# Kernel optimization log

Measured on AMD Instinct MI355X. Metric: run time of the kernel, lower is better.

Reference implementation:

```python
import jax, jax.numpy as jnp
import numpy as np

NEG_INF = -1e10  # matches the -10000000000.0 additive mask in the torch source


def setup_inputs() -> dict:
    key = jax.random.key(0)
    k1, k2, k3, k4 = jax.random.split(key, 4)
    bs, h, S, d = 4, 16, 2048, 64
    bs_h = bs * h
    query = jax.random.normal(k1, (bs_h, S, d), dtype=jnp.float32)
    key_t = jax.random.normal(k2, (bs_h, S, d), dtype=jnp.float32)
    value = jax.random.normal(k3, (bs_h, S, d), dtype=jnp.float32)
    attn_mask = jax.random.randint(k4, (bs, S), 0, 2).astype(jnp.int32)
    return {"query": query, "key": key_t, "value": value,
            "attn_mask": attn_mask, "decod_mask": 1}


def reference(query, key, value, attn_mask, decod_mask):
    bs_h, K, d_k = key.shape
    Q = query.shape[1]
    bs = attn_mask.shape[0]
    h = bs_h // bs

    # scores: [bs_h, Q, K]
    scores = jnp.einsum('bqd,bkd->bqk', query, key) / jnp.sqrt(
        jnp.asarray(d_k, dtype=query.dtype))

    # padding mask: positions where attn_mask == 0 get -1e10.
    # torch repeats the [bs, Q, K] mask h times along the batch axis
    # (order: [mask; mask; ...]), i.e. batch index b in bs_h maps to b % bs.
    pad = (attn_mask == 0).astype(scores.dtype) * NEG_INF  # [bs, K]
    scores = (scores.reshape(h, bs, Q, K) + pad[None, :, None, :]).reshape(bs_h, Q, K)

    if decod_mask is not None:
        causal = jnp.triu(jnp.full((Q, K), NEG_INF, dtype=scores.dtype), k=1)
        scores = scores + causal[None, :, :]

    attn = jax.nn.softmax(scores, axis=-1)
    # dropout p=0.0 -> identity
    return jnp.einsum('bqk,bkd->bqd', attn, value)
```

## Files before the change

kernel.cpp:

```cpp
#include <hip/hip_runtime.h>
#include <hip/hip_bf16.h>

#define S_LEN 2048
#define DH 64
#define NBATCH 4
#define LOG2E 1.44269504088896f
#define SCL2E 0.18033688011112042f
#define PADC  (-1.44269504088896e10f)
#define NEG_BIG -1e10f
#define NEG_CAUSAL -3.0e38f

typedef __attribute__((ext_vector_type(8))) short short8;
typedef __attribute__((ext_vector_type(4))) float floatx4;
typedef __attribute__((ext_vector_type(4))) unsigned uintx4;

__device__ inline float fast_exp2(float x) {
#if __has_builtin(__builtin_amdgcn_exp2f)
  return __builtin_amdgcn_exp2f(x);
#else
  return exp2f(x);
#endif
}

__device__ inline short f2bf(float x) {
  union { float f; unsigned u; } v; v.f = x;
  unsigned r = v.u + 0x7fffu + ((v.u >> 16) & 1u);
  return (short)(r >> 16);
}

__device__ inline short8 pack8(float4 a, float4 b) {
  short8 r;
  r[0] = f2bf(a.x); r[1] = f2bf(a.y); r[2] = f2bf(a.z); r[3] = f2bf(a.w);
  r[4] = f2bf(b.x); r[5] = f2bf(b.y); r[6] = f2bf(b.z); r[7] = f2bf(b.w);
  return r;
}

__device__ inline unsigned packhi(unsigned hi, unsigned lo) {
#if __has_builtin(__builtin_amdgcn_perm)
  return __builtin_amdgcn_perm(hi, lo, 0x07060302u);
#else
  return (hi & 0xFFFF0000u) | (lo >> 16);
#endif
}

#define MFMA32(a, b, c) __builtin_amdgcn_mfma_f32_16x16x32_bf16(a, b, c, 0, 0, 0)

__global__ void prep_kv(const float* __restrict__ Kg, const float* __restrict__ Vg,
                        short8* __restrict__ Kf, short8* __restrict__ Vf) {
  const int gid = (int)blockIdx.x;
  if (gid < 4096) {
    const int idx = gid * 256 + (int)threadIdx.x;
    const int lane = idx & 63;
    const int t = idx >> 6;
    const int nt = t & 3, ks = (t >> 2) & 1;
    const int kt = (t >> 3) & 31;
    const int bh = t >> 8;
    const int c = lane & 15, g = lane >> 4;
    const float* src = Kg + ((size_t)bh * S_LEN + kt * 64 + nt * 16 + c) * DH + ks * 32 + g * 8;
    float4 a = *(const float4*)src;
    float4 b = *(const float4*)(src + 4);
    Kf[idx] = pack8(a, b);
  } else {
    const int idx = (gid - 4096) * 256 + (int)threadIdx.x;
    const int lane = idx & 63;
    const int t = idx >> 6;
    const int dt = t & 3, nt2 = (t >> 2) & 1;
    const int kt = (t >> 3) & 31;
    const int bh = t >> 8;
    const int c = lane & 15, g = lane >> 4;
    const int key0 = kt * 64 + nt2 * 32 + g * 4;
    const float* src = Vg + ((size_t)bh * S_LEN + key0) * DH + dt * 16 + c;
    short8 r;
#pragma unroll
    for (int j = 0; j < 4; ++j) r[j] = f2bf(src[(size_t)j * DH]);
#pragma unroll
    for (int j = 0; j < 4; ++j) r[4 + j] = f2bf(src[(size_t)(16 + j) * DH]);
    Vf[idx] = r;
  }
}

__global__ __launch_bounds__(256, 2) void flash_fwd2(
    const float* __restrict__ Qg, const int* __restrict__ maskg,
    const short8* __restrict__ KfB, const short8* __restrict__ VfB,
    float* __restrict__ Og)
{
  const int bh = blockIdx.x;
  const int qt = 15 - (int)blockIdx.y;
  const int b  = bh & (NBATCH - 1);
  const int tid = (int)threadIdx.x;
  const int w = tid >> 6, lane = tid & 63;
  const int c = lane & 15, g = lane >> 4;
  const int qbase = qt * 128 + w * 32;

  const short8 ones = {0x3F80, 0x3F80, 0x3F80, 0x3F80, 0x3F80, 0x3F80, 0x3F80, 0x3F80};

  short8 qf[2][2];
#pragma unroll
  for (int s2 = 0; s2 < 2; ++s2) {
    const float* qp = Qg + ((size_t)bh * S_LEN + qbase + s2 * 16 + c) * DH + g * 8;
#pragma unroll
    for (int ks = 0; ks < 2; ++ks) {
      float4 a  = *(const float4*)(qp + ks * 32);
      float4 b4 = *(const float4*)(qp + ks * 32 + 4);
      qf[s2][ks] = pack8(a, b4);
    }
  }

  floatx4 acc[2][4];
  floatx4 acc_l[2];
#pragma unroll
  for (int s2 = 0; s2 < 2; ++s2) {
    acc_l[s2] = (floatx4){0.f, 0.f, 0.f, 0.f};
#pragma unroll
    for (int dt = 0; dt < 4; ++dt) acc[s2][dt] = (floatx4){0.f, 0.f, 0.f, 0.f};
  }

  const int ktmax = 2 * qt + 1;
  for (int kt = 0; kt <= ktmax; ++kt) {
    const short8* kfp = KfB + ((size_t)(bh * 32 + kt) * 8) * 64 + lane;
    short8 kf[2][4];
#pragma unroll
    for (int ks = 0; ks < 2; ++ks)
#pragma unroll
      for (int nt = 0; nt < 4; ++nt) kf[ks][nt] = kfp[(ks * 4 + nt) * 64];

    const short8* vfp = VfB + ((size_t)(bh * 32 + kt) * 8) * 64 + lane;
    short8 vf[2][4];
#pragma unroll
    for (int nt2 = 0; nt2 < 2; ++nt2)
#pragma unroll
      for (int dt = 0; dt < 4; ++dt) vf[nt2][dt] = vfp[(nt2 * 4 + dt) * 64];

    floatx4 padv[4];
#pragma unroll
    for (int nt = 0; nt < 4; ++nt) {
      int4 mv = *(const int4*)&maskg[b * S_LEN + kt * 64 + nt * 16 + g * 4];
      padv[nt][0] = mv.x ? 0.f : PADC;
      padv[nt][1] = mv.y ? 0.f : PADC;
      padv[nt][2] = mv.z ? 0.f : PADC;
      padv[nt][3] = mv.w ? 0.f : PADC;
    }

#pragma unroll
    for (int s2 = 0; s2 < 2; ++s2) {
      if (kt * 64 > qbase + s2 * 16 + 15) continue;
      floatx4 st[4];
#pragma unroll
      for (int nt = 0; nt < 4; ++nt) {
        floatx4 cc = (floatx4){0.f, 0.f, 0.f, 0.f};
        cc = MFMA32(kf[0][nt], qf[s2][0], cc);
        cc = MFMA32(kf[1][nt], qf[s2][1], cc);
        st[nt] = cc;
      }
      const int q = qbase + s2 * 16 + c;
      const bool causal = (kt * 64 + 63) > (qbase + s2 * 16);
      unsigned pu[4][4];
#pragma unroll
      for (int nt = 0; nt < 4; ++nt) {
#pragma unroll
        for (int r = 0; r < 4; ++r) {
          float arg = fmaf(st[nt][r], SCL2E, padv[nt][r]);
          if (causal) {
            const int key = kt * 64 + nt * 16 + g * 4 + r;
            arg = (key > q) ? NEG_CAUSAL : arg;
          }
          pu[nt][r] = __float_as_uint(fast_exp2(arg)) + 0x8000u;
        }
      }
      short8 pP[2];
#pragma unroll
      for (int nt2 = 0; nt2 < 2; ++nt2) {
        uintx4 wv;
        wv[0] = packhi(pu[2 * nt2][1],     pu[2 * nt2][0]);
        wv[1] = packhi(pu[2 * nt2][3],     pu[2 * nt2][2]);
        wv[2] = packhi(pu[2 * nt2 + 1][1], pu[2 * nt2 + 1][0]);
        wv[3] = packhi(pu[2 * nt2 + 1][3], pu[2 * nt2 + 1][2]);
        pP[nt2] = __builtin_bit_cast(short8, wv);
      }
#pragma unroll
      for (int nt2 = 0; nt2 < 2; ++nt2) {
        acc_l[s2] = MFMA32(pP[nt2], ones, acc_l[s2]);
#pragma unroll
        for (int dt = 0; dt < 4; ++dt)
          acc[s2][dt] = MFMA32(pP[nt2], vf[nt2][dt], acc[s2][dt]);
      }
    }
  }

#pragma unroll
  for (int s2 = 0; s2 < 2; ++s2) {
    float rr[4];
#pragma unroll
    for (int r = 0; r < 4; ++r) rr[r] = 1.f / acc_l[s2][r];
#pragma unroll
    for (int dt = 0; dt < 4; ++dt)
#pragma unroll
      for (int r = 0; r < 4; ++r)
        Og[((size_t)bh * S_LEN + qbase + s2 * 16 + g * 4 + r) * DH + dt * 16 + c] =
            acc[s2][dt][r] * rr[r];
  }
}

__global__ __launch_bounds__(256, 2) void flash_fwd_lds(
    const float* __restrict__ Qg, const float* __restrict__ Kg,
    const float* __restrict__ Vg, const int* __restrict__ maskg,
    float* __restrict__ Og)
{
  const int qt  = blockIdx.x;
  const int bh  = blockIdx.y;
  const int b   = bh & (NBATCH - 1);
  const int tid = (int)threadIdx.x;
  const int w = tid >> 6, lane = tid & 63;
  const int g = lane >> 4, c = lane & 15;

  __shared__ __align__(16) short Ks[64 * 72];
  __shared__ __align__(16) short Vt[64 * 72];
  __shared__ __align__(16) short Ps[4][32 * 72];

  short8 qf[2][2];
#pragma unroll
  for (int s2 = 0; s2 < 2; ++s2) {
    const float* qp = Qg + ((size_t)bh * S_LEN + qt * 128 + w * 32 + s2 * 16 + c) * DH + g * 8;
#pragma unroll
    for (int ks = 0; ks < 2; ++ks) {
      float4 a  = *(const float4*)(qp + ks * 32);
      float4 bq = *(const float4*)(qp + ks * 32 + 4);
      qf[s2][ks] = pack8(a, bq);
    }
  }

  floatx4 acc[2][4];
  float mrow[2][4], lrow[2][4];
#pragma unroll
  for (int s2 = 0; s2 < 2; ++s2) {
#pragma unroll
    for (int i = 0; i < 4; ++i) acc[s2][i] = (floatx4){0.f, 0.f, 0.f, 0.f};
#pragma unroll
    for (int r = 0; r < 4; ++r) { mrow[s2][r] = -3.4e38f; lrow[s2][r] = 0.f; }
  }

  const int rstage = tid >> 2;
  const int dstage = (tid & 3) * 16;
  const int ktmax = 2 * qt + 1;

  for (int kt = 0; kt <= ktmax; ++kt) {
    __syncthreads();
    {
      const size_t rowbase = ((size_t)bh * S_LEN + kt * 64 + rstage) * DH + dstage;
      const float* kp = Kg + rowbase;
      const float* vp = Vg + rowbase;
      float4 k0 = *(const float4*)kp;       float4 k1 = *(const float4*)(kp + 4);
      float4 k2 = *(const float4*)(kp + 8); float4 k3 = *(const float4*)(kp + 12);
      *(short8*)&Ks[rstage * 72 + dstage]     = pack8(k0, k1);
      *(short8*)&Ks[rstage * 72 + dstage + 8] = pack8(k2, k3);
      float4 v0 = *(const float4*)vp;       float4 v1 = *(const float4*)(vp + 4);
      float4 v2 = *(const float4*)(vp + 8); float4 v3 = *(const float4*)(vp + 12);
      float vv[16] = {v0.x, v0.y, v0.z, v0.w, v1.x, v1.y, v1.z, v1.w,
                      v2.x, v2.y, v2.z, v2.w, v3.x, v3.y, v3.z, v3.w};
#pragma unroll
      for (int i = 0; i < 16; ++i) Vt[(dstage + i) * 72 + rstage] = f2bf(vv[i]);
    }
    __syncthreads();

    float padv[4];
#pragma unroll
    for (int nt = 0; nt < 4; ++nt)
      padv[nt] = (maskg[b * S_LEN + kt * 64 + nt * 16 + c] != 0) ? 0.f : NEG_BIG;

    short8 kf[2][4];
#pragma unroll
    for (int ks = 0; ks < 2; ++ks)
#pragma unroll
      for (int nt = 0; nt < 4; ++nt)
        kf[ks][nt] = *(const short8*)&Ks[(nt * 16 + c) * 72 + ks * 32 + g * 8];

    bool act[2];
#pragma unroll
    for (int s2 = 0; s2 < 2; ++s2)
      act[s2] = (kt * 64) <= (qt * 128 + w * 32 + s2 * 16 + 15);

#pragma unroll
    for (int s2 = 0; s2 < 2; ++s2) {
      if (!act[s2]) continue;
      floatx4 sv[4];
#pragma unroll
      for (int nt = 0; nt < 4; ++nt) {
        floatx4 cc = (floatx4){0.f, 0.f, 0.f, 0.f};
        cc = MFMA32(qf[s2][0], kf[0][nt], cc);
        cc = MFMA32(qf[s2][1], kf[1][nt], cc);
        sv[nt] = cc;
      }
      const int qrow0 = qt * 128 + w * 32 + s2 * 16 + g * 4;
#pragma unroll
      for (int nt = 0; nt < 4; ++nt) {
        const int key = kt * 64 + nt * 16 + c;
#pragma unroll
        for (int r = 0; r < 4; ++r) {
          float s = sv[nt][r] * 0.125f + padv[nt];
          if (key > qrow0 + r) s = NEG_CAUSAL;
          sv[nt][r] = s;
        }
      }
#pragma unroll
      for (int r = 0; r < 4; ++r) {
        float mx = fmaxf(fmaxf(sv[0][r], sv[1][r]), fmaxf(sv[2][r], sv[3][r]));
        mx = fmaxf(mx, __shfl_xor(mx, 1));
        mx = fmaxf(mx, __shfl_xor(mx, 2));
        mx = fmaxf(mx, __shfl_xor(mx, 4));
        mx = fmaxf(mx, __shfl_xor(mx, 8));
        const float mold = mrow[s2][r];
        const float mnew = fmaxf(mold, mx);
        const float corr = fast_exp2((mold - mnew) * LOG2E);
        float ps = 0.f;
#pragma unroll
        for (int nt = 0; nt < 4; ++nt) {
          float p = fast_exp2((sv[nt][r] - mnew) * LOG2E);
          sv[nt][r] = p;
          ps += p;
        }
        ps += __shfl_xor(ps, 1);
        ps += __shfl_xor(ps, 2);
        ps += __shfl_xor(ps, 4);
        ps += __shfl_xor(ps, 8);
        lrow[s2][r] = lrow[s2][r] * corr + ps;
        mrow[s2][r] = mnew;
#pragma unroll
        for (int dt = 0; dt < 4; ++dt) acc[s2][dt][r] *= corr;
      }
#pragma unroll
      for (int nt = 0; nt < 4; ++nt)
#pragma unroll
        for (int r = 0; r < 4; ++r)
          Ps[w][(s2 * 16 + g * 4 + r) * 72 + nt * 16 + c] = f2bf(sv[nt][r]);
    }

#pragma unroll
    for (int ks = 0; ks < 2; ++ks) {
      short8 pf0 = {}, pf1 = {};
      if (act[0]) pf0 = *(const short8*)&Ps[w][c * 72 + ks * 32 + g * 8];
      if (act[1]) pf1 = *(const short8*)&Ps[w][(16 + c) * 72 + ks * 32 + g * 8];
#pragma unroll
      for (int dt = 0; dt < 4; ++dt) {
        short8 vfr = *(const short8*)&Vt[(dt * 16 + c) * 72 + ks * 32 + g * 8];
        if (act[0]) acc[0][dt] = MFMA32(pf0, vfr, acc[0][dt]);
        if (act[1]) acc[1][dt] = MFMA32(pf1, vfr, acc[1][dt]);
      }
    }
  }

#pragma unroll
  for (int s2 = 0; s2 < 2; ++s2) {
    float rl[4];
#pragma unroll
    for (int r = 0; r < 4; ++r) rl[r] = 1.f / lrow[s2][r];
    const size_t obase = ((size_t)bh * S_LEN + qt * 128 + w * 32 + s2 * 16 + g * 4) * DH + c;
#pragma unroll
    for (int dt = 0; dt < 4; ++dt)
#pragma unroll
      for (int r = 0; r < 4; ++r)
        Og[obase + (size_t)r * DH + dt * 16] = acc[s2][dt][r] * rl[r];
  }
}

__global__ void fixup(const float* __restrict__ Vg, const int* __restrict__ maskg,
                      float* __restrict__ Og)
{
  const int bh = blockIdx.x;
  const int b  = bh & (NBATCH - 1);
  const int tid = (int)threadIdx.x;
  __shared__ int sFirst;
  __shared__ float4 sRed[64][16];
  __shared__ int sCnt[64];
  if (tid == 0) sFirst = S_LEN;
  __syncthreads();
  for (int k = tid; k < S_LEN; k += 1024)
    if (maskg[b * S_LEN + k] != 0) atomicMin(&sFirst, k);
  __syncthreads();
  const int f = sFirst;
  if (f == 0) return;

  const int dq = tid & 15, kg = tid >> 4;
  float4 a = {0.f, 0.f, 0.f, 0.f}; int cnt = 0;
  for (int k = kg; k < S_LEN; k += 64) {
    if (maskg[b * S_LEN + k] != 0) {
      float4 v = *(const float4*)&Vg[((size_t)bh * S_LEN + k) * DH + dq * 4];
      a.x += v.x; a.y += v.y; a.z += v.z; a.w += v.w; cnt++;
    }
  }
  sRed[kg][dq] = a;
  if (dq == 0) sCnt[kg] = cnt;
  __syncthreads();
  if (tid < 64) {
    const int q4 = tid >> 2, e = tid & 3;
    float ms = 0.f; int n = 0;
#pragma unroll 4
    for (int i = 0; i < 64; ++i) {
      const float* p4 = (const float*)&sRed[i][q4];
      ms += p4[e];
      n += sCnt[i];
    }
    float pre = 0.f;
    for (int q = 0; q < f; ++q) {
      pre += Vg[((size_t)bh * S_LEN + q) * DH + tid];
      Og[((size_t)bh * S_LEN + q) * DH + tid] = (pre + ms) / (float)(q + 1 + n);
    }
  }
}

extern "C" void kernel_launch(void* const* d_in, const int* in_sizes, int n_in,
                              void* d_out, int out_size, void* d_ws, size_t ws_size,
                              hipStream_t stream) {
  const float* Q = (const float*)d_in[0];
  const float* K = (const float*)d_in[1];
  const float* V = (const float*)d_in[2];
  const int* mask = (const int*)d_in[3];
  float* O = (float*)d_out;

  const size_t KF_BYTES = (size_t)64 * S_LEN * DH * 2;
  if (ws_size >= 2 * KF_BYTES) {
    short8* Kf = (short8*)d_ws;
    short8* Vf = (short8*)((char*)d_ws + KF_BYTES);
    prep_kv<<<dim3(8192), dim3(256), 0, stream>>>(K, V, Kf, Vf);
    flash_fwd2<<<dim3(64, 16), dim3(256), 0, stream>>>(Q, mask, Kf, Vf, O);
  } else {
    flash_fwd_lds<<<dim3(16, 64), dim3(256), 0, stream>>>(Q, K, V, mask, O);
  }
  fixup<<<dim3(64), dim3(1024), 0, stream>>>(V, mask, O);
}
```

Before: 222.0 us.

## Double-buffer K/V tiles in LDS via async global_load_lds with MFMA priority hints

Each workgroup now stages its K/V tiles into double-buffered shared memory using global_load_lds. Each wave copies one quarter of the next tile while the current tile is computed from LDS, with a barrier per iteration. Before, every wave read the same K/V fragments directly from global memory. This is meant to remove the redundant global traffic across the four waves and to overlap the loads with compute. It also wraps the MFMA sections in s_setprio. The risks are the added barrier per tile, which is problematic with per-wave causal early-outs, and a possible missing vmcnt wait before the barrier. It also adds 32KB of LDS per block, which could affect occupancy. It is unclear whether flash_fwd2 is the kernel launched by default.

```diff
diff --git a/kernel.cpp b/kernel.cpp
--- a/kernel.cpp
+++ b/kernel.cpp
@@ -44,6 +44,19 @@
 }
 
 #define MFMA32(a, b, c) __builtin_amdgcn_mfma_f32_16x16x32_bf16(a, b, c, 0, 0, 0)
+
+typedef __attribute__((address_space(1))) void __gas1_v;
+typedef __attribute__((address_space(3))) void __gas3_v;
+__device__ __forceinline__ void gload16(const void* g, void* l) {
+  __builtin_amdgcn_global_load_lds((__gas1_v*)g, (__gas3_v*)l, 16, 0, 0);
+}
+
+__device__ __forceinline__ void stage_chunk(const short8* src_base, short8* dst_base,
+                                            int lane) {
+#pragma unroll
+  for (int i = 0; i < 4; ++i)
+    gload16((const void*)(src_base + i * 64 + lane), (void*)(dst_base + i * 64));
+}
 
 __global__ void prep_kv(const float* __restrict__ Kg, const float* __restrict__ Vg,
                         short8* __restrict__ Kf, short8* __restrict__ Vf) {
@@ -92,6 +105,9 @@
   const int c = lane & 15, g = lane >> 4;
   const int qbase = qt * 128 + w * 32;
 
+  __shared__ short8 sK[2][512];
+  __shared__ short8 sV[2][512];
+
   const short8 ones = {0x3F80, 0x3F80, 0x3F80, 0x3F80, 0x3F80, 0x3F80, 0x3F80, 0x3F80};
 
   short8 qf[2][2];
@@ -115,36 +131,56 @@
     for (int dt = 0; dt < 4; ++dt) acc[s2][dt] = (floatx4){0.f, 0.f, 0.f, 0.f};
   }
 
+  const short8* gsel = (w & 2) ? (VfB + (size_t)bh * 32 * 512)
+                               : (KfB + (size_t)bh * 32 * 512);
+  const int half = (w & 1) * 256;
+
   const int ktmax = 2 * qt + 1;
+
+  {
+    short8* dsel = (w & 2) ? sV[0] : sK[0];
+    stage_chunk(gsel + half, dsel + half, lane);
+  }
+  __syncthreads();
+
+  int cur = 0;
   for (int kt = 0; kt <= ktmax; ++kt) {
-    const short8* kfp = KfB + ((size_t)(bh * 32 + kt) * 8) * 64 + lane;
+    int4 mv[4];
+#pragma unroll
+    for (int nt = 0; nt < 4; ++nt)
+      mv[nt] = *(const int4*)&maskg[b * S_LEN + kt * 64 + nt * 16 + g * 4];
+
+    if (kt < ktmax) {
+      short8* dsel = (w & 2) ? sV[cur ^ 1] : sK[cur ^ 1];
+      stage_chunk(gsel + (size_t)(kt + 1) * 512 + half, dsel + half, lane);
+    }
+
+    floatx4 padv[4];
+#pragma unroll
+    for (int nt = 0; nt < 4; ++nt) {
+      padv[nt][0] = mv[nt].x ? 0.f : PADC;
+      padv[nt][1] = mv[nt].y ? 0.f : PADC;
+      padv[nt][2] = mv[nt].z ? 0.f : PADC;
+      padv[nt][3] = mv[nt].w ? 0.f : PADC;
+    }
+
     short8 kf[2][4];
 #pragma unroll
     for (int ks = 0; ks < 2; ++ks)
 #pragma unroll
-      for (int nt = 0; nt < 4; ++nt) kf[ks][nt] = kfp[(ks * 4 + nt) * 64];
-
-    const short8* vfp = VfB + ((size_t)(bh * 32 + kt) * 8) * 64 + lane;
+      for (int nt = 0; nt < 4; ++nt) kf[ks][nt] = sK[cur][(ks * 4 + nt) * 64 + lane];
+
     short8 vf[2][4];
 #pragma unroll
     for (int nt2 = 0; nt2 < 2; ++nt2)
 #pragma unroll
-      for (int dt = 0; dt < 4; ++dt) vf[nt2][dt] = vfp[(nt2 * 4 + dt) * 64];
-
-    floatx4 padv[4];
-#pragma unroll
-    for (int nt = 0; nt < 4; ++nt) {
-      int4 mv = *(const int4*)&maskg[b * S_LEN + kt * 64 + nt * 16 + g * 4];
-      padv[nt][0] = mv.x ? 0.f : PADC;
-      padv[nt][1] = mv.y ? 0.f : PADC;
-      padv[nt][2] = mv.z ? 0.f : PADC;
-      padv[nt][3] = mv.w ? 0.f : PADC;
-    }
+      for (int dt = 0; dt < 4; ++dt) vf[nt2][dt] = sV[cur][(nt2 * 4 + dt) * 64 + lane];
 
 #pragma unroll
     for (int s2 = 0; s2 < 2; ++s2) {
       if (kt * 64 > qbase + s2 * 16 + 15) continue;
       floatx4 st[4];
+      __builtin_amdgcn_s_setprio(1);
 #pragma unroll
       for (int nt = 0; nt < 4; ++nt) {
         floatx4 cc = (floatx4){0.f, 0.f, 0.f, 0.f};
@@ -152,6 +188,7 @@
         cc = MFMA32(kf[1][nt], qf[s2][1], cc);
         st[nt] = cc;
       }
+      __builtin_amdgcn_s_setprio(0);
       const int q = qbase + s2 * 16 + c;
       const bool causal = (kt * 64 + 63) > (qbase + s2 * 16);
       unsigned pu[4][4];
@@ -177,6 +214,7 @@
         wv[3] = packhi(pu[2 * nt2 + 1][3], pu[2 * nt2 + 1][2]);
         pP[nt2] = __builtin_bit_cast(short8, wv);
       }
+      __builtin_amdgcn_s_setprio(1);
 #pragma unroll
       for (int nt2 = 0; nt2 < 2; ++nt2) {
         acc_l[s2] = MFMA32(pP[nt2], ones, acc_l[s2]);
@@ -184,6 +222,12 @@
         for (int dt = 0; dt < 4; ++dt)
           acc[s2][dt] = MFMA32(pP[nt2], vf[nt2][dt], acc[s2][dt]);
       }
+      __builtin_amdgcn_s_setprio(0);
+    }
+
+    if (kt < ktmax) {
+      __syncthreads();
+      cur ^= 1;
     }
   }
 
```

After: 223.4 us. No clear change (+0.6%).

## Balance causal work per wave, double-buffer K fragments, fold masked V sums into prep

Applied to the files above, without the earlier changes.

Each wave now processes two 32-row query chunks taken from opposite ends of the sequence (widx and 63-widx), so causal work per wave is balanced and the grid halves. K fragments are double-buffered in registers, loading the next tile while the current one computes, and s_setprio is raised around the MFMA blocks. The masked-V column sums used by the fully-masked-row fixup are now accumulated with atomics inside prep_kv, replacing the heavier fixup kernel with a lighter fixup_write. The trade-offs are more register pressure, an extra zeroing launch, and float atomics whose summation order is nondeterministic.

```diff
diff --git a/kernel.cpp b/kernel.cpp
--- a/kernel.cpp
+++ b/kernel.cpp
@@ -45,8 +45,13 @@
 
 #define MFMA32(a, b, c) __builtin_amdgcn_mfma_f32_16x16x32_bf16(a, b, c, 0, 0, 0)
 
+__global__ void zero_sums(float* __restrict__ s) {
+  s[blockIdx.x * 256 + threadIdx.x] = 0.f;
+}
+
 __global__ void prep_kv(const float* __restrict__ Kg, const float* __restrict__ Vg,
-                        short8* __restrict__ Kf, short8* __restrict__ Vf) {
+                        short8* __restrict__ Kf, short8* __restrict__ Vf,
+                        const int* __restrict__ maskg, float* __restrict__ sums) {
   const int gid = (int)blockIdx.x;
   if (gid < 4096) {
     const int idx = gid * 256 + (int)threadIdx.x;
@@ -67,137 +72,208 @@
     const int dt = t & 3, nt2 = (t >> 2) & 1;
     const int kt = (t >> 3) & 31;
     const int bh = t >> 8;
+    const int b = bh & (NBATCH - 1);
     const int c = lane & 15, g = lane >> 4;
     const int key0 = kt * 64 + nt2 * 32 + g * 4;
     const float* src = Vg + ((size_t)bh * S_LEN + key0) * DH + dt * 16 + c;
+    int4 m0 = *(const int4*)&maskg[b * S_LEN + key0];
+    int4 m1 = *(const int4*)&maskg[b * S_LEN + key0 + 16];
     short8 r;
-#pragma unroll
-    for (int j = 0; j < 4; ++j) r[j] = f2bf(src[(size_t)j * DH]);
-#pragma unroll
-    for (int j = 0; j < 4; ++j) r[4 + j] = f2bf(src[(size_t)(16 + j) * DH]);
+    float s = 0.f;
+    {
+      float v0 = src[(size_t)0 * DH], v1 = src[(size_t)1 * DH];
+      float v2 = src[(size_t)2 * DH], v3 = src[(size_t)3 * DH];
+      r[0] = f2bf(v0); r[1] = f2bf(v1); r[2] = f2bf(v2); r[3] = f2bf(v3);
+      s += (m0.x ? v0 : 0.f) + (m0.y ? v1 : 0.f) + (m0.z ? v2 : 0.f) + (m0.w ? v3 : 0.f);
+    }
+    {
+      float v0 = src[(size_t)16 * DH], v1 = src[(size_t)17 * DH];
+      float v2 = src[(size_t)18 * DH], v3 = src[(size_t)19 * DH];
+      r[4] = f2bf(v0); r[5] = f2bf(v1); r[6] = f2bf(v2); r[7] = f2bf(v3);
+      s += (m1.x ? v0 : 0.f) + (m1.y ? v1 : 0.f) + (m1.z ? v2 : 0.f) + (m1.w ? v3 : 0.f);
+    }
     Vf[idx] = r;
-  }
-}
-
-__global__ __launch_bounds__(256, 2) void flash_fwd2(
+    s += __shfl_xor(s, 16);
+    s += __shfl_xor(s, 32);
+    if (lane < 16) atomicAdd(&sums[bh * 64 + dt * 16 + lane], s);
+  }
+}
+
+__device__ __forceinline__ void loadk(const short8* __restrict__ kbase, int kt,
+                                      int lane, short8 (&dst)[8]) {
+  const short8* p = kbase + ((size_t)kt * 8) * 64 + lane;
+#pragma unroll
+  for (int i = 0; i < 8; ++i) dst[i] = p[i * 64];
+}
+
+__device__ __forceinline__ void compute_tile(
+    int kt, int qbase, int b, int c, int g, int lane,
+    const short8 (&kf)[8], const short8 (&qf)[2][2], const short8& ones,
+    const int* __restrict__ maskg, const short8* __restrict__ vbase,
+    floatx4 (&acc)[2][4], floatx4 (&acc_l)[2])
+{
+  int4 mv[4];
+#pragma unroll
+  for (int nt = 0; nt < 4; ++nt)
+    mv[nt] = *(const int4*)&maskg[b * S_LEN + kt * 64 + nt * 16 + g * 4];
+
+  short8 vf[8];
+  {
+    const short8* vp = vbase + ((size_t)kt * 8) * 64 + lane;
+#pragma unroll
+    for (int i = 0; i < 8; ++i) vf[i] = vp[i * 64];
+  }
+
+  floatx4 padv[4];
+#pragma unroll
+  for (int nt = 0; nt < 4; ++nt) {
+    padv[nt][0] = mv[nt].x ? 0.f : PADC;
+    padv[nt][1] = mv[nt].y ? 0.f : PADC;
+    padv[nt][2] = mv[nt].z ? 0.f : PADC;
+    padv[nt][3] = mv[nt].w ? 0.f : PADC;
+  }
+
+#pragma unroll
+  for (int s2 = 0; s2 < 2; ++s2) {
+    if (kt * 64 > qbase + s2 * 16 + 15) continue;
+    floatx4 st[4];
+    __builtin_amdgcn_s_setprio(1);
+#pragma unroll
+    for (int nt = 0; nt < 4; ++nt) {
+      floatx4 cc = (floatx4){0.f, 0.f, 0.f, 0.f};
+      cc = MFMA32(kf[nt],     qf[s2][0], cc);
+      cc = MFMA32(kf[4 + nt], qf[s2][1], cc);
+      st[nt] = cc;
+    }
+    __builtin_amdgcn_s_setprio(0);
+    const int q = qbase + s2 * 16 + c;
+    const bool causal = (kt * 64 + 63) > (qbase + s2 * 16);
+    unsigned pu[4][4];
+#pragma unroll
+    for (int nt = 0; nt < 4; ++nt) {
+#pragma unroll
+      for (int r = 0; r < 4; ++r) {
+        float arg = fmaf(st[nt][r], SCL2E, padv[nt][r]);
+        if (causal) {
+          const int key = kt * 64 + nt * 16 + g * 4 + r;
+          arg = (key > q) ? NEG_CAUSAL : arg;
+        }
+        pu[nt][r] = __float_as_uint(fast_exp2(arg)) + 0x8000u;
+      }
+    }
+    short8 pP[2];
+#pragma unroll
+    for (int nt2 = 0; nt2 < 2; ++nt2) {
+      uintx4 wv;
+      wv[0] = packhi(pu[2 * nt2][1],     pu[2 * nt2][0]);
+      wv[1] = packhi(pu[2 * nt2][3],     pu[2 * nt2][2]);
+      wv[2] = packhi(pu[2 * nt2 + 1][1], pu[2 * nt2 + 1][0]);
+      wv[3] = packhi(pu[2 * nt2 + 1][3], pu[2 * nt2 + 1][2]);
+      pP[nt2] = __builtin_bit_cast(short8, wv);
+    }
+    __builtin_amdgcn_s_setprio(1);
+#pragma unroll
+    for (int nt2 = 0; nt2 < 2; ++nt2) {
+      acc_l[s2] = MFMA32(pP[nt2], ones, acc_l[s2]);
+#pragma unroll
+      for (int dt = 0; dt < 4; ++dt)
+        acc[s2][dt] = MFMA32(pP[nt2], vf[nt2 * 4 + dt], acc[s2][dt]);
+    }
+    __builtin_amdgcn_s_setprio(0);
+  }
+}
+
+__global__ __launch_bounds__(256, 2) void flash_fwd3(
     const float* __restrict__ Qg, const int* __restrict__ maskg,
     const short8* __restrict__ KfB, const short8* __restrict__ VfB,
     float* __restrict__ Og)
 {
   const int bh = blockIdx.x;
-  const int qt = 15 - (int)blockIdx.y;
   const int b  = bh & (NBATCH - 1);
   const int tid = (int)threadIdx.x;
   const int w = tid >> 6, lane = tid & 63;
+  const int widx = (int)blockIdx.y * 4 + w;
   const int c = lane & 15, g = lane >> 4;
-  const int qbase = qt * 128 + w * 32;
 
   const short8 ones = {0x3F80, 0x3F80, 0x3F80, 0x3F80, 0x3F80, 0x3F80, 0x3F80, 0x3F80};
-
-  short8 qf[2][2];
-#pragma unroll
-  for (int s2 = 0; s2 < 2; ++s2) {
-    const float* qp = Qg + ((size_t)bh * S_LEN + qbase + s2 * 16 + c) * DH + g * 8;
-#pragma unroll
-    for (int ks = 0; ks < 2; ++ks) {
-      float4 a  = *(const float4*)(qp + ks * 32);
-      float4 b4 = *(const float4*)(qp + ks * 32 + 4);
-      qf[s2][ks] = pack8(a, b4);
-    }
-  }
-
-  floatx4 acc[2][4];
-  floatx4 acc_l[2];
-#pragma unroll
-  for (int s2 = 0; s2 < 2; ++s2) {
-    acc_l[s2] = (floatx4){0.f, 0.f, 0.f, 0.f};
-#pragma unroll
-    for (int dt = 0; dt < 4; ++dt) acc[s2][dt] = (floatx4){0.f, 0.f, 0.f, 0.f};
-  }
-
-  const int ktmax = 2 * qt + 1;
-  for (int kt = 0; kt <= ktmax; ++kt) {
-    const short8* kfp = KfB + ((size_t)(bh * 32 + kt) * 8) * 64 + lane;
-    short8 kf[2][4];
-#pragma unroll
-    for (int ks = 0; ks < 2; ++ks)
-#pragma unroll
-      for (int nt = 0; nt < 4; ++nt) kf[ks][nt] = kfp[(ks * 4 + nt) * 64];
-
-    const short8* vfp = VfB + ((size_t)(bh * 32 + kt) * 8) * 64 + lane;
-    short8 vf[2][4];
-#pragma unroll
-    for (int nt2 = 0; nt2 < 2; ++nt2)
-#pragma unroll
-      for (int dt = 0; dt < 4; ++dt) vf[nt2][dt] = vfp[(nt2 * 4 + dt) * 64];
-
-    floatx4 padv[4];
-#pragma unroll
-    for (int nt = 0; nt < 4; ++nt) {
-      int4 mv = *(const int4*)&maskg[b * S_LEN + kt * 64 + nt * 16 + g * 4];
-      padv[nt][0] = mv.x ? 0.f : PADC;
-      padv[nt][1] = mv.y ? 0.f : PADC;
-      padv[nt][2] = mv.z ? 0.f : PADC;
-      padv[nt][3] = mv.w ? 0.f : PADC;
-    }
-
+  const short8* kbase = KfB + (size_t)bh * 32 * 8 * 64;
+  const short8* vbase = VfB + (size_t)bh * 32 * 8 * 64;
+
+#pragma unroll
+  for (int half = 0; half < 2; ++half) {
+    const int ch = half ? (63 - widx) : widx;
+    const int qbase = ch * 32;
+    const int ktmax = ch >> 1;
+
+    short8 qf[2][2];
 #pragma unroll
     for (int s2 = 0; s2 < 2; ++s2) {
-      if (kt * 64 > qbase + s2 * 16 + 15) continue;
-      floatx4 st[4];
-#pragma unroll
-      for (int nt = 0; nt < 4; ++nt) {
-        floatx4 cc = (floatx4){0.f, 0.f, 0.f, 0.f};
-        cc = MFMA32(kf[0][nt], qf[s2][0], cc);
-        cc = MFMA32(kf[1][nt], qf[s2][1], cc);
-        st[nt] = cc;
-      }
-      const int q = qbase + s2 * 16 + c;
-      const bool causal = (kt * 64 + 63) > (qbase + s2 * 16);
-      unsigned pu[4][4];
-#pragma unroll
-      for (int nt = 0; nt < 4; ++nt) {
-#pragma unroll
-        for (int r = 0; r < 4; ++r) {
-          float arg = fmaf(st[nt][r], SCL2E, padv[nt][r]);
-          if (causal) {
-            const int key = kt * 64 + nt * 16 + g * 4 + r;
-            arg = (key > q) ? NEG_CAUSAL : arg;
-          }
-          pu[nt][r] = __float_as_uint(fast_exp2(arg)) + 0x8000u;
-        }
-      }
-      short8 pP[2];
-#pragma unroll
-      for (int nt2 = 0; nt2 < 2; ++nt2) {
-        uintx4 wv;
-        wv[0] = packhi(pu[2 * nt2][1],     pu[2 * nt2][0]);
-        wv[1] = packhi(pu[2 * nt2][3],     pu[2 * nt2][2]);
-        wv[2] = packhi(pu[2 * nt2 + 1][1], pu[2 * nt2 + 1][0]);
-        wv[3] = packhi(pu[2 * nt2 + 1][3], pu[2 * nt2 + 1][2]);
-        pP[nt2] = __builtin_bit_cast(short8, wv);
-      }
-#pragma unroll
-      for (int nt2 = 0; nt2 < 2; ++nt2) {
-        acc_l[s2] = MFMA32(pP[nt2], ones, acc_l[s2]);
-#pragma unroll
-        for (int dt = 0; dt < 4; ++dt)
-          acc[s2][dt] = MFMA32(pP[nt2], vf[nt2][dt], acc[s2][dt]);
-      }
-    }
-  }
-
-#pragma unroll
-  for (int s2 = 0; s2 < 2; ++s2) {
-    float rr[4];
-#pragma unroll
-    for (int r = 0; r < 4; ++r) rr[r] = 1.f / acc_l[s2][r];
-#pragma unroll
-    for (int dt = 0; dt < 4; ++dt)
-#pragma unroll
-      for (int r = 0; r < 4; ++r)
-        Og[((size_t)bh * S_LEN + qbase + s2 * 16 + g * 4 + r) * DH + dt * 16 + c] =
-            acc[s2][dt][r] * rr[r];
+      const float* qp = Qg + ((size_t)bh * S_LEN + qbase + s2 * 16 + c) * DH + g * 8;
+#pragma unroll
+      for (int ks = 0; ks < 2; ++ks) {
+        float4 a  = *(const float4*)(qp + ks * 32);
+        float4 b4 = *(const float4*)(qp + ks * 32 + 4);
+        qf[s2][ks] = pack8(a, b4);
+      }
+    }
+
+    floatx4 acc[2][4];
+    floatx4 acc_l[2];
+#pragma unroll
+    for (int s2 = 0; s2 < 2; ++s2) {
+      acc_l[s2] = (floatx4){0.f, 0.f, 0.f, 0.f};
+#pragma unroll
+      for (int dt = 0; dt < 4; ++dt) acc[s2][dt] = (floatx4){0.f, 0.f, 0.f, 0.f};
+    }
+
+    short8 kfA[8], kfB_[8];
+    loadk(kbase, 0, lane, kfA);
+    for (int kt = 0; kt <= ktmax; kt += 2) {
+      const bool hasB = (kt + 1 <= ktmax);
+      if (hasB) loadk(kbase, kt + 1, lane, kfB_);
+      compute_tile(kt, qbase, b, c, g, lane, kfA, qf, ones, maskg, vbase, acc, acc_l);
+      if (hasB) {
+        if (kt + 2 <= ktmax) loadk(kbase, kt + 2, lane, kfA);
+        compute_tile(kt + 1, qbase, b, c, g, lane, kfB_, qf, ones, maskg, vbase, acc, acc_l);
+      }
+    }
+
+#pragma unroll
+    for (int s2 = 0; s2 < 2; ++s2) {
+      float rr[4];
+#pragma unroll
+      for (int r = 0; r < 4; ++r) rr[r] = 1.f / acc_l[s2][r];
+#pragma unroll
+      for (int dt = 0; dt < 4; ++dt)
+#pragma unroll
+        for (int r = 0; r < 4; ++r)
+          Og[((size_t)bh * S_LEN + qbase + s2 * 16 + g * 4 + r) * DH + dt * 16 + c] =
+              acc[s2][dt][r] * rr[r];
+    }
+  }
+}
+
+__global__ void fixup_write(const float* __restrict__ Vg, const int* __restrict__ maskg,
+                            const float* __restrict__ sums, float* __restrict__ Og)
+{
+  const int bh = blockIdx.x;
+  const int b  = bh & (NBATCH - 1);
+  const int d  = (int)threadIdx.x;
+  int fmin = S_LEN, n = 0;
+  for (int k = d; k < S_LEN; k += 64) {
+    if (maskg[b * S_LEN + k] != 0) { ++n; if (k < fmin) fmin = k; }
+  }
+#pragma unroll
+  for (int off = 1; off < 64; off <<= 1) {
+    fmin = min(fmin, __shfl_xor(fmin, off));
+    n += __shfl_xor(n, off);
+  }
+  if (fmin == 0) return;
+  const float ms = sums[bh * 64 + d];
+  float pre = 0.f;
+  for (int q = 0; q < fmin; ++q) {
+    pre += Vg[((size_t)bh * S_LEN + q) * DH + d];
+    Og[((size_t)bh * S_LEN + q) * DH + d] = (pre + ms) / (float)(q + 1 + n);
   }
 }
 
@@ -417,13 +493,17 @@
   float* O = (float*)d_out;
 
   const size_t KF_BYTES = (size_t)64 * S_LEN * DH * 2;
-  if (ws_size >= 2 * KF_BYTES) {
+  const size_t SUM_BYTES = (size_t)64 * 64 * sizeof(float);
+  if (ws_size >= 2 * KF_BYTES + SUM_BYTES) {
     short8* Kf = (short8*)d_ws;
     short8* Vf = (short8*)((char*)d_ws + KF_BYTES);
-    prep_kv<<<dim3(8192), dim3(256), 0, stream>>>(K, V, Kf, Vf);
-    flash_fwd2<<<dim3(64, 16), dim3(256), 0, stream>>>(Q, mask, Kf, Vf, O);
+    float* sums = (float*)((char*)d_ws + 2 * KF_BYTES);
+    zero_sums<<<dim3(16), dim3(256), 0, stream>>>(sums);
+    prep_kv<<<dim3(8192), dim3(256), 0, stream>>>(K, V, Kf, Vf, mask, sums);
+    flash_fwd3<<<dim3(64, 8), dim3(256), 0, stream>>>(Q, mask, Kf, Vf, O);
+    fixup_write<<<dim3(64), dim3(64), 0, stream>>>(V, mask, sums, O);
   } else {
     flash_fwd_lds<<<dim3(16, 64), dim3(256), 0, stream>>>(Q, K, V, mask, O);
-  }
-  fixup<<<dim3(64), dim3(1024), 0, stream>>>(V, mask, O);
-}
+    fixup<<<dim3(64), dim3(1024), 0, stream>>>(V, mask, O);
+  }
+}
```

New measurement: 203.2 us. 8.4% less time.
